# Kernel optimization log

Measured on AMD Instinct MI355X. Metric: run time of the kernel, lower is better.

The kernel has to match this reference:

```python
import jax, jax.numpy as jnp
import numpy as np

TOPK = 10
MIN_SIM = 0.8
MIN_VOTES = 0.0
REMOVE_INNER_THR = 0.8
NUM_CLASSES = 1000
D, C, N = 256, 256, 500000


def setup_inputs() -> dict:
    key = jax.random.key(0)
    k1, k2, k3, k4, k5 = jax.random.split(key, 5)
    # query descriptors, L2-normalized (cosine similarity, matches min_sim=0.8 semantics)
    q = jax.random.normal(k1, (D, C), dtype=jnp.float32)
    q = q / jnp.linalg.norm(q, axis=1, keepdims=True)
    # database descriptors + integer place_id stored as the last float column
    x = jax.random.normal(k2, (N, C), dtype=jnp.float32)
    x = x / jnp.linalg.norm(x, axis=1, keepdims=True)
    ids = jax.random.randint(k3, (N,), 0, NUM_CLASSES).astype(jnp.float32)
    places_db = jnp.concatenate([x, ids[:, None]], axis=1)  # (N, C+1)
    # valid xyxy boxes in a ~1000px image
    xy = jax.random.uniform(k4, (D, 2), dtype=jnp.float32) * 800.0
    wh = jax.random.uniform(k5, (D, 2), dtype=jnp.float32) * 200.0 + 1.0
    final_boxes = jnp.concatenate([xy, xy + wh], axis=1)  # (D, 4)
    return {"final_boxes": final_boxes, "descriptors": q, "places_db": places_db}


def _remove_overlapping_boxes(boxes, labels, thr):
    # boxes: (D,4) xyxy, labels: (D,) int32
    b = boxes.astype(jnp.float32)
    areas = (b[:, 2] - b[:, 0]) * (b[:, 3] - b[:, 1])  # (D,)
    xi1 = jnp.maximum(b[:, None, 0], b[None, :, 0])
    yi1 = jnp.maximum(b[:, None, 1], b[None, :, 1])
    xi2 = jnp.minimum(b[:, None, 2], b[None, :, 2])
    yi2 = jnp.minimum(b[:, None, 3], b[None, :, 3])
    inter = jnp.clip(xi2 - xi1, 0.0) * jnp.clip(yi2 - yi1, 0.0)  # (D,D)
    area_i = areas[:, None]
    area_j = areas[None, :]
    area_small = jnp.minimum(area_i, area_j)
    overlap = jnp.where(area_small > 0, inter / jnp.where(area_small > 0, area_small, 1.0), 0.0)
    same_lbl = (labels[:, None] == labels[None, :]) & (labels[:, None] >= 0)
    n = boxes.shape[0]
    non_diag = ~jnp.eye(n, dtype=bool)
    mask_pair = same_lbl & (overlap >= thr) & non_diag
    bigger_i = area_i > area_j
    remove_i = jnp.any(mask_pair & bigger_i, axis=1)
    remove_j = jnp.any(mask_pair & ~bigger_i, axis=0)
    remove = remove_i | remove_j
    return jnp.where(remove, jnp.full_like(labels, -1), labels)


def reference(final_boxes, descriptors, places_db):
    X = places_db[:, :-1]                       # (N, C)
    idx = places_db[:, -1].astype(jnp.int32)    # (N,)
    sims = descriptors @ X.T                    # (D, N)
    top_sims, top_idx = jax.lax.top_k(sims, TOPK)  # (D, K)
    top_ids = idx[top_idx]                      # (D, K)
    mask_sim = top_sims >= MIN_SIM              # (D, K)
    one_hot = jax.nn.one_hot(top_ids, NUM_CLASSES, dtype=jnp.float32)  # (D, K, Ncls)
    vote_counts = jnp.sum(one_hot * mask_sim[..., None].astype(jnp.float32), axis=1)  # (D, Ncls)
    majority_counts = jnp.max(vote_counts, axis=1)
    majority_ids = jnp.argmax(vote_counts, axis=1).astype(jnp.int32)
    valid_votes = jnp.sum(mask_sim, axis=1).astype(jnp.float32)
    vote_ratio = jnp.where(valid_votes > 0, majority_counts / jnp.where(valid_votes > 0, valid_votes, 1.0), 0.0)
    valid = (majority_counts > 0) & (vote_ratio >= MIN_VOTES)
    results = jnp.where(valid, majority_ids, jnp.full_like(majority_ids, -1))
    results = _remove_overlapping_boxes(final_boxes, results, REMOVE_INNER_THR)
    match = (top_ids == results[:, None]) & mask_sim
    sim_scores = jnp.max(jnp.where(match, top_sims, jnp.zeros_like(top_sims)), axis=1)  # (D,)
    return (final_boxes, sim_scores, results)
```

## Files before the change

### kernel.cpp

```cpp
#include <hip/hip_runtime.h>
#include <stdint.h>

#define NQ      256
#define NC      256
#define NDB     500000
#define ROWLEN  257
#define MIN_SIM_F 0.8f
#define NMS_THR   0.8f
#define CAP     64
#define TILE    32
#define NTILES  (NDB / TILE)
#define BLK     512
#define GEMM_GRID 512

typedef __bf16 bf16x8 __attribute__((ext_vector_type(8)));
typedef float  f32x4  __attribute__((ext_vector_type(4)));

union BU { unsigned short u[8]; bf16x8 v; };

__device__ __forceinline__ unsigned short f2bf(float f) {
    uint32_t u = __float_as_uint(f);
    u += 0x7FFFu + ((u >> 16) & 1u);
    return (unsigned short)(u >> 16);
}

__global__ void init_counts(int* cnt) { cnt[threadIdx.x] = 0; }

__global__ __launch_bounds__(BLK, 4) void gemm_filter(
    const float* __restrict__ q, const float* __restrict__ db,
    int* __restrict__ cnt, float* __restrict__ csim, int* __restrict__ cidx)
{
    __shared__ __align__(16) unsigned short Bs[2][TILE][264];

    const int tid  = threadIdx.x;
    const int wave = tid >> 6;
    const int lane = tid & 63;
    const int quad = lane >> 4;
    const int l16  = lane & 15;
    const int rrow = tid >> 4;
    const int jcol = tid & 15;

    bf16x8 a[2][8];
    #pragma unroll
    for (int f = 0; f < 2; ++f) {
        const int m = wave * 32 + f * 16 + l16;
        const float* qrow = q + m * NC;
        #pragma unroll
        for (int s = 0; s < 8; ++s) {
            const int k0 = s * 32 + quad * 8;
            BU u;
            #pragma unroll
            for (int j = 0; j < 8; ++j) u.u[j] = f2bf(qrow[k0 + j]);
            a[f][s] = u.v;
        }
    }

    f32x4 p0, p1, p2, p3;

    auto LOAD = [&](int tile) {
        const float* s = db + ((size_t)tile * TILE + rrow) * ROWLEN + jcol * 16;
        p0 = *(const f32x4*)(s + 0);
        p1 = *(const f32x4*)(s + 4);
        p2 = *(const f32x4*)(s + 8);
        p3 = *(const f32x4*)(s + 12);
    };

    auto WRITE = [&](int nb) {
        union { unsigned short u[8]; uint4 v; } w0, w1;
        #pragma unroll
        for (int e = 0; e < 4; ++e) {
            w0.u[e]     = f2bf(p0[e]);
            w0.u[4 + e] = f2bf(p1[e]);
            w1.u[e]     = f2bf(p2[e]);
            w1.u[4 + e] = f2bf(p3[e]);
        }
        uint4* dst = (uint4*)&Bs[nb][rrow][jcol * 16];
        dst[0] = w0.v;
        dst[1] = w1.v;
    };

    auto COMPUTE = [&](int cb, int tile) {
        const f32x4 zero = {0.f, 0.f, 0.f, 0.f};
        f32x4 acc[2][2] = {{zero, zero}, {zero, zero}};
        #pragma unroll
        for (int s = 0; s < 8; ++s) {
            const bf16x8 b0 = *(const bf16x8*)&Bs[cb][l16][s * 32 + quad * 8];
            const bf16x8 b1 = *(const bf16x8*)&Bs[cb][16 + l16][s * 32 + quad * 8];
            acc[0][0] = __builtin_amdgcn_mfma_f32_16x16x32_bf16(a[0][s], b0, acc[0][0], 0, 0, 0);
            acc[1][0] = __builtin_amdgcn_mfma_f32_16x16x32_bf16(a[1][s], b0, acc[1][0], 0, 0, 0);
            acc[0][1] = __builtin_amdgcn_mfma_f32_16x16x32_bf16(a[0][s], b1, acc[0][1], 0, 0, 0);
            acc[1][1] = __builtin_amdgcn_mfma_f32_16x16x32_bf16(a[1][s], b1, acc[1][1], 0, 0, 0);
        }
        float mx = acc[0][0][0];
        #pragma unroll
        for (int fm = 0; fm < 2; ++fm)
            #pragma unroll
            for (int h = 0; h < 2; ++h)
                #pragma unroll
                for (int rr = 0; rr < 4; ++rr) mx = fmaxf(mx, acc[fm][h][rr]);
        if (mx >= MIN_SIM_F) {
            #pragma unroll
            for (int fm = 0; fm < 2; ++fm) {
                #pragma unroll
                for (int h = 0; h < 2; ++h) {
                    #pragma unroll
                    for (int rr = 0; rr < 4; ++rr) {
                        const float sv = acc[fm][h][rr];
                        if (sv >= MIN_SIM_F) {
                            const int qi   = wave * 32 + fm * 16 + quad * 4 + rr;
                            const int rowg = tile * TILE + h * 16 + l16;
                            const int pos = atomicAdd(&cnt[qi], 1);
                            if (pos < CAP) {
                                csim[qi * CAP + pos] = sv;
                                cidx[qi * CAP + pos] = rowg;
                            }
                        }
                    }
                }
            }
        }
    };

    int tile = blockIdx.x;
    LOAD(tile);
    WRITE(0);
    __syncthreads();
    int buf = 0;
    for (;;) {
        const int next = tile + GEMM_GRID;
        const bool more = (next < NTILES);
        if (more) LOAD(next);
        COMPUTE(buf, tile);
        if (!more) break;
        WRITE(buf ^ 1);
        __syncthreads();
        buf ^= 1;
        tile = next;
    }
}

__device__ __forceinline__ bool better(float s1, int i1, float s2, int i2) {
    return (s1 > s2) || (s1 == s2 && i1 < i2);
}

__global__ __launch_bounds__(256) void postprocess(
    const float* __restrict__ boxes, const float* __restrict__ db,
    const int* __restrict__ cnt, const float* __restrict__ csim,
    const int* __restrict__ cidx, float* __restrict__ out)
{
    __shared__ int   lab[NQ];
    __shared__ float area_s[NQ];
    __shared__ float bx[NQ][4];

    const int q = threadIdx.x;

    float s10[10]; int i10[10];
    int k = 0;
    int c = cnt[q]; if (c > CAP) c = CAP;
    for (int j = 0; j < c; ++j) {
        const float s = csim[q * CAP + j];
        const int   ix = cidx[q * CAP + j];
        int p;
        if (k < 10) { p = k; ++k; }
        else { if (!better(s, ix, s10[9], i10[9])) continue; p = 9; }
        while (p > 0 && better(s, ix, s10[p - 1], i10[p - 1])) {
            s10[p] = s10[p - 1]; i10[p] = i10[p - 1]; --p;
        }
        s10[p] = s; i10[p] = ix;
    }

    int vid[10];
    for (int j = 0; j < k; ++j) vid[j] = (int)db[(size_t)i10[j] * ROWLEN + (ROWLEN - 1)];
    int best_cnt = 0, best_id = 0x7fffffff;
    for (int j = 0; j < k; ++j) {
        int cj = 0;
        for (int l = 0; l < k; ++l) cj += (vid[l] == vid[j]) ? 1 : 0;
        if (cj > best_cnt || (cj == best_cnt && vid[j] < best_id)) { best_cnt = cj; best_id = vid[j]; }
    }
    const int lq = (best_cnt > 0) ? best_id : -1;
    lab[q] = lq;

    const float x1 = boxes[q * 4 + 0], y1 = boxes[q * 4 + 1];
    const float x2 = boxes[q * 4 + 2], y2 = boxes[q * 4 + 3];
    bx[q][0] = x1; bx[q][1] = y1; bx[q][2] = x2; bx[q][3] = y2;
    const float aq = (x2 - x1) * (y2 - y1);
    area_s[q] = aq;
    __syncthreads();

    bool rem = false;
    if (lq >= 0) {
        for (int p = 0; p < NQ; ++p) {
            if (p == q || lab[p] != lq) continue;
            const float ap = area_s[p];
            if (ap > aq) continue;
            const float xi1 = fmaxf(x1, bx[p][0]);
            const float yi1 = fmaxf(y1, bx[p][1]);
            const float xi2 = fminf(x2, bx[p][2]);
            const float yi2 = fminf(y2, bx[p][3]);
            const float inter = fmaxf(xi2 - xi1, 0.f) * fmaxf(yi2 - yi1, 0.f);
            const float small = fminf(aq, ap);
            const float ov = (small > 0.f) ? inter / small : 0.f;
            if (ov >= NMS_THR) { rem = true; break; }
        }
    }
    const int lq2 = rem ? -1 : lq;

    float score = 0.f;
    if (lq2 >= 0)
        for (int j = 0; j < k; ++j)
            if (vid[j] == lq2) score = fmaxf(score, s10[j]);

    for (int t = q; t < NQ * 4; t += NQ) out[t] = boxes[t];
    out[NQ * 4 + q] = score;
    out[NQ * 5 + q] = (float)lq2;
}

extern "C" void kernel_launch(void* const* d_in, const int* in_sizes, int n_in,
                              void* d_out, int out_size, void* d_ws, size_t ws_size,
                              hipStream_t stream) {
    const float* boxes = (const float*)d_in[0];
    const float* desc  = (const float*)d_in[1];
    const float* db    = (const float*)d_in[2];
    float* out = (float*)d_out;

    int*   cnt  = (int*)d_ws;
    float* csim = (float*)((char*)d_ws + 1024);
    int*   cidx = (int*)((char*)d_ws + 1024 + NQ * CAP * 4);

    init_counts<<<1, 256, 0, stream>>>(cnt);
    gemm_filter<<<GEMM_GRID, BLK, 0, stream>>>(desc, db, cnt, csim, cidx);
    postprocess<<<1, 256, 0, stream>>>(boxes, db, cnt, csim, cidx, out);
}
```

Measured before the change: 656.5 us.

## Coalesce database row loads per wave and deepen the prefetch pipeline

Each wave now loads whole database rows, with lanes reading consecutive 4-float chunks, instead of each thread reading 16 contiguous floats from a quarter-row. This gives fully contiguous 1 KB accesses per wave instruction. The main loop now writes the prefetched tile to shared memory before compute and issues the global load for the tile after that, so two tiles are in flight. The query load is also vectorized. In exchange, more registers stay live across compute and the shared-memory stores become narrower 8-byte writes.

After: 681.0 us. +3.7%, slower.

```diff
diff --git a/kernel.cpp b/kernel.cpp
--- a/kernel.cpp
+++ b/kernel.cpp
@@ -15,6 +15,7 @@
 
 typedef __bf16 bf16x8 __attribute__((ext_vector_type(8)));
 typedef float  f32x4  __attribute__((ext_vector_type(4)));
+typedef float  f32x4u __attribute__((ext_vector_type(4), aligned(4)));
 
 union BU { unsigned short u[8]; bf16x8 v; };
 
@@ -37,8 +38,6 @@
     const int lane = tid & 63;
     const int quad = lane >> 4;
     const int l16  = lane & 15;
-    const int rrow = tid >> 4;
-    const int jcol = tid & 15;
 
     bf16x8 a[2][8];
     #pragma unroll
@@ -48,35 +47,41 @@
         #pragma unroll
         for (int s = 0; s < 8; ++s) {
             const int k0 = s * 32 + quad * 8;
+            const f32x4 v0 = *(const f32x4*)(qrow + k0);
+            const f32x4 v1 = *(const f32x4*)(qrow + k0 + 4);
             BU u;
             #pragma unroll
-            for (int j = 0; j < 8; ++j) u.u[j] = f2bf(qrow[k0 + j]);
+            for (int j = 0; j < 4; ++j) {
+                u.u[j]     = f2bf(v0[j]);
+                u.u[4 + j] = f2bf(v1[j]);
+            }
             a[f][s] = u.v;
         }
     }
 
     f32x4 p0, p1, p2, p3;
 
-    auto LOAD = [&](int tile) {
-        const float* s = db + ((size_t)tile * TILE + rrow) * ROWLEN + jcol * 16;
-        p0 = *(const f32x4*)(s + 0);
-        p1 = *(const f32x4*)(s + 4);
-        p2 = *(const f32x4*)(s + 8);
-        p3 = *(const f32x4*)(s + 12);
+    auto LOAD4 = [&](int tile) {
+        const float* base = db + (size_t)tile * TILE * ROWLEN + (size_t)lane * 4;
+        p0 = *(const f32x4u*)(base + (size_t)(wave)      * ROWLEN);
+        p1 = *(const f32x4u*)(base + (size_t)(8 + wave)  * ROWLEN);
+        p2 = *(const f32x4u*)(base + (size_t)(16 + wave) * ROWLEN);
+        p3 = *(const f32x4u*)(base + (size_t)(24 + wave) * ROWLEN);
     };
 
-    auto WRITE = [&](int nb) {
-        union { unsigned short u[8]; uint4 v; } w0, w1;
+    auto WRITE4 = [&](int nb) {
+        union { unsigned short u[4]; uint2 v; } w0, w1, w2, w3;
         #pragma unroll
         for (int e = 0; e < 4; ++e) {
-            w0.u[e]     = f2bf(p0[e]);
-            w0.u[4 + e] = f2bf(p1[e]);
-            w1.u[e]     = f2bf(p2[e]);
-            w1.u[4 + e] = f2bf(p3[e]);
-        }
-        uint4* dst = (uint4*)&Bs[nb][rrow][jcol * 16];
-        dst[0] = w0.v;
-        dst[1] = w1.v;
+            w0.u[e] = f2bf(p0[e]);
+            w1.u[e] = f2bf(p1[e]);
+            w2.u[e] = f2bf(p2[e]);
+            w3.u[e] = f2bf(p3[e]);
+        }
+        *(uint2*)&Bs[nb][wave][lane * 4]      = w0.v;
+        *(uint2*)&Bs[nb][8 + wave][lane * 4]  = w1.v;
+        *(uint2*)&Bs[nb][16 + wave][lane * 4] = w2.v;
+        *(uint2*)&Bs[nb][24 + wave][lane * 4] = w3.v;
     };
 
     auto COMPUTE = [&](int cb, int tile) {
@@ -122,20 +127,23 @@
     };
 
     int tile = blockIdx.x;
-    LOAD(tile);
-    WRITE(0);
+    LOAD4(tile);
+    WRITE4(0);
+    int nxt = tile + GEMM_GRID;
+    bool havep = (nxt < NTILES);
+    if (havep) LOAD4(nxt);
     __syncthreads();
-    int buf = 0;
+    int bi = 0;
+
     for (;;) {
-        const int next = tile + GEMM_GRID;
-        const bool more = (next < NTILES);
-        if (more) LOAD(next);
-        COMPUTE(buf, tile);
-        if (!more) break;
-        WRITE(buf ^ 1);
+        if (havep) WRITE4(bi ^ 1);
+        const int  n2    = nxt + GEMM_GRID;
+        const bool have2 = havep && (n2 < NTILES);
+        if (have2) LOAD4(n2);
+        COMPUTE(bi, tile);
+        if (!havep) break;
         __syncthreads();
-        buf ^= 1;
-        tile = next;
+        tile = nxt; nxt = n2; havep = have2; bi ^= 1;
     }
 }
 
```
